# Optimization experiments

Measured on AMD Instinct MI355X. Metric: run time of the kernel, lower is better.

The kernel has to match this reference:

```python
import jax, jax.numpy as jnp
import numpy as np

NUM_TOKENS = 131072
INPUT_DIM = 1024
NUM_EXPERTS = 8
TOP_K = 2


def setup_inputs() -> dict:
    key = jax.random.key(0)
    kx, kw, kb = jax.random.split(key, 3)
    x = jax.random.normal(kx, (NUM_TOKENS, INPUT_DIM), dtype=jnp.float32)
    # nn.Linear(input_dim, num_experts): W [E, D], b [E]
    lim = 1.0 / np.sqrt(INPUT_DIM)
    W = jax.random.uniform(kw, (NUM_EXPERTS, INPUT_DIM), dtype=jnp.float32, minval=-lim, maxval=lim)
    b = jax.random.uniform(kb, (NUM_EXPERTS,), dtype=jnp.float32, minval=-lim, maxval=lim)
    return {"x": x, "W": W, "b": b}


def reference(x, W, b):
    # gating_scores = gate(x): [N, E]
    logits = jnp.einsum('nd,ed->ne', x, W) + b
    probs = jax.nn.softmax(logits, axis=1)
    # torch.topk returns (values, indices); module returns (indices, values)
    top_k_values, top_k_indices = jax.lax.top_k(probs, TOP_K)
    return (top_k_indices, top_k_values)
```

## Files before the change

kernel.cpp:

```cpp
#include <hip/hip_runtime.h>
#include <math.h>


#define NUM_TOKENS 131072
#define DIM        1024
#define NE         8
#define TPB        256
#define DC         64
#define ROWSTRIDE  68

__global__ __launch_bounds__(TPB)
void topk_gating_kernel(const float* __restrict__ x,
                        const float* __restrict__ W,
                        const float* __restrict__ b,
                        float* __restrict__ out)
{
    __shared__ float lds[TPB * ROWSTRIDE];
    const int t    = threadIdx.x;
    const int tok0 = blockIdx.x * TPB;

    float acc[NE];
#pragma unroll
    for (int e = 0; e < NE; ++e) acc[e] = 0.f;

    const float4* x4   = (const float4*)x;
    const float4* W4   = (const float4*)W;
    float4*       lds4 = (float4*)lds;

    for (int c = 0; c < DIM / DC; ++c) {
        __syncthreads();
#pragma unroll
        for (int l = 0; l < 16; ++l) {
            int flat = l * TPB + t;
            int r    = flat >> 4;
            int c4   = flat & 15;
            float4 v = x4[(tok0 + r) * (DIM / 4) + c * (DC / 4) + c4];
            lds4[r * (ROWSTRIDE / 4) + c4] = v;
        }
        __syncthreads();
#pragma unroll 4
        for (int j = 0; j < DC / 4; ++j) {
            float4 xv = lds4[t * (ROWSTRIDE / 4) + j];
            int d = c * (DC / 4) + j;
#pragma unroll
            for (int e = 0; e < NE; ++e) {
                float4 w = W4[e * (DIM / 4) + d];
                acc[e] = fmaf(xv.x, w.x, acc[e]);
                acc[e] = fmaf(xv.y, w.y, acc[e]);
                acc[e] = fmaf(xv.z, w.z, acc[e]);
                acc[e] = fmaf(xv.w, w.w, acc[e]);
            }
        }
    }

    float logit[NE];
#pragma unroll
    for (int e = 0; e < NE; ++e) logit[e] = acc[e] + b[e];

    float v1 = -INFINITY, v2 = -INFINITY;
    int   i1 = 0,         i2 = 0;
#pragma unroll
    for (int e = 0; e < NE; ++e) {
        float v = logit[e];
        if (v > v1)      { v2 = v1; i2 = i1; v1 = v; i1 = e; }
        else if (v > v2) { v2 = v;  i2 = e; }
    }

    float sum = 0.f;
#pragma unroll
    for (int e = 0; e < NE; ++e) sum += __expf(logit[e] - v1);
    float inv = 1.0f / sum;
    float p1  = inv;
    float p2  = __expf(v2 - v1) * inv;

    int n = tok0 + t;
    float2* outi = (float2*)out;
    float2* outv = (float2*)(out + 2 * (size_t)NUM_TOKENS);
    outi[n] = make_float2((float)i1, (float)i2);
    outv[n] = make_float2(p1, p2);
}

extern "C" void kernel_launch(void* const* d_in, const int* in_sizes, int n_in,
                              void* d_out, int out_size, void* d_ws, size_t ws_size,
                              hipStream_t stream) {
    const float* x = (const float*)d_in[0];
    const float* W = (const float*)d_in[1];
    const float* b = (const float*)d_in[2];
    float* out = (float*)d_out;

    dim3 grid(NUM_TOKENS / TPB);
    dim3 block(TPB);
    topk_gating_kernel<<<grid, block, 0, stream>>>(x, W, b, out);
}
```

Before: 781.6 us.

## Per-wave LDS transpose with register prefetch of next x chunk, drop block barriers

Each wave now stages its own 64 tokens in a private LDS region, so the block-wide __syncthreads are removed. The next 64-float chunk of x is prefetched into registers while the current chunk is being computed, which overlaps global loads with FMA work. Launch bounds now ask for two blocks per CU. The cost is 16 float4 prefetch registers per thread, which raises register pressure. Intra-wave LDS ordering relies on the implicit lockstep of the wave, with no explicit barrier.

Result: slower. 903.9 us (+15.7%).

```diff
diff --git a/kernel.cpp b/kernel.cpp
--- a/kernel.cpp
+++ b/kernel.cpp
@@ -4,47 +4,65 @@
 
 #define NUM_TOKENS 131072
 #define DIM        1024
+#define D4         (DIM / 4)
 #define NE         8
 #define TPB        256
+#define TOKW       64
 #define DC         64
-#define ROWSTRIDE  68
+#define DC4        (DC / 4)
+#define NCHUNK     (DIM / DC)
+#define RS4        17
 
-__global__ __launch_bounds__(TPB)
+__global__ __launch_bounds__(TPB, 2)
 void topk_gating_kernel(const float* __restrict__ x,
                         const float* __restrict__ W,
                         const float* __restrict__ b,
                         float* __restrict__ out)
 {
-    __shared__ float lds[TPB * ROWSTRIDE];
+    __shared__ float4 lds4[4 * TOKW * RS4];
+
     const int t    = threadIdx.x;
-    const int tok0 = blockIdx.x * TPB;
+    const int wave = t >> 6;
+    const int lane = t & 63;
+    const int wtok0 = blockIdx.x * TPB + wave * TOKW;
+    float4* wb4 = lds4 + wave * TOKW * RS4;
+
+    const float4* x4 = (const float4*)x;
+    const float4* W4 = (const float4*)W;
+
+    const int h  = lane >> 4;
+    const int lo = lane & 15;
 
     float acc[NE];
 #pragma unroll
     for (int e = 0; e < NE; ++e) acc[e] = 0.f;
 
-    const float4* x4   = (const float4*)x;
-    const float4* W4   = (const float4*)W;
-    float4*       lds4 = (float4*)lds;
+    float4 pf[16];
+#pragma unroll
+    for (int q = 0; q < 16; ++q) {
+        int r = q * 4 + h;
+        pf[q] = x4[(size_t)(wtok0 + r) * D4 + lo];
+    }
 
-    for (int c = 0; c < DIM / DC; ++c) {
-        __syncthreads();
+    for (int c = 0; c < NCHUNK; ++c) {
 #pragma unroll
-        for (int l = 0; l < 16; ++l) {
-            int flat = l * TPB + t;
-            int r    = flat >> 4;
-            int c4   = flat & 15;
-            float4 v = x4[(tok0 + r) * (DIM / 4) + c * (DC / 4) + c4];
-            lds4[r * (ROWSTRIDE / 4) + c4] = v;
+        for (int q = 0; q < 16; ++q) {
+            int r = q * 4 + h;
+            wb4[r * RS4 + lo] = pf[q];
         }
-        __syncthreads();
-#pragma unroll 4
-        for (int j = 0; j < DC / 4; ++j) {
-            float4 xv = lds4[t * (ROWSTRIDE / 4) + j];
-            int d = c * (DC / 4) + j;
+        if (c + 1 < NCHUNK) {
+#pragma unroll
+            for (int q = 0; q < 16; ++q) {
+                int r = q * 4 + h;
+                pf[q] = x4[(size_t)(wtok0 + r) * D4 + (c + 1) * DC4 + lo];
+            }
+        }
+#pragma unroll
+        for (int j = 0; j < DC4; ++j) {
+            float4 xv = wb4[lane * RS4 + j];
 #pragma unroll
             for (int e = 0; e < NE; ++e) {
-                float4 w = W4[e * (DIM / 4) + d];
+                float4 w = W4[e * D4 + c * DC4 + j];
                 acc[e] = fmaf(xv.x, w.x, acc[e]);
                 acc[e] = fmaf(xv.y, w.y, acc[e]);
                 acc[e] = fmaf(xv.z, w.z, acc[e]);
@@ -73,7 +91,7 @@
     float p1  = inv;
     float p2  = __expf(v2 - v1) * inv;
 
-    int n = tok0 + t;
+    int n = wtok0 + lane;
     float2* outi = (float2*)out;
     float2* outv = (float2*)(out + 2 * (size_t)NUM_TOKENS);
     outi[n] = make_float2((float)i1, (float)i2);
```
